# Optimization experiments

Measured on AMD Instinct MI355X. Metric: run time of the kernel, lower is better.

Reference implementation:

```python
import jax, jax.numpy as jnp
import numpy as np
from jax import lax

N_LAYERS = 10  # Sinkhorn(n_layers=10)


def setup_inputs() -> dict:
    key = jax.random.key(0)
    k1, k2, k3 = jax.random.split(key, 3)
    S, NA, NB = 4, 4096, 4096
    alpha = jax.random.uniform(k1, (S, NA), jnp.float32, 0.05, 1.0)
    alpha = alpha / alpha.sum(-1, keepdims=True)  # probability simplex
    beta = jax.random.uniform(k2, (S, NB), jnp.float32, 0.05, 1.0)
    beta = beta / beta.sum(-1, keepdims=True)
    C = jax.random.uniform(k3, (NA, NB), jnp.float32)  # nonneg cost matrix
    eps = jnp.float32(0.1)  # entropic regularization
    return {"alpha": alpha, "beta": beta, "C": C, "eps": eps}


def reference(alpha, beta, C, eps):
    # Log-domain Sinkhorn: f,g are dual potentials, shapes (S,NA)/(S,NB).
    log_alpha = jnp.log(alpha)
    log_beta = jnp.log(beta)

    def log_dot_exp(A, b):
        # A: (n, m), b: (S, m) -> (S, n); matches torch log_dot_exp (2D case)
        return jax.scipy.special.logsumexp((-A[None, :, :] + b[:, None, :]) / eps, axis=-1)

    def step(carry, _):
        _, g = carry
        f = eps * (log_alpha - log_dot_exp(C, g))
        g = eps * (log_beta - log_dot_exp(C.T, f))
        return (f, g), None

    f0 = jnp.zeros_like(alpha)
    g0 = jnp.zeros_like(beta)
    (f, g), _ = lax.scan(step, (f0, g0), None, length=N_LAYERS)
    return f, g
```

## Files before the change

### kernel.cpp

```cpp
#include <hip/hip_runtime.h>
#include <stdint.h>

#define NN 4096
#define NITER 10
#define ROWS 16
#define NBLK 256

#define STG_OFF  131072
#define RED_OFF  147712

static __device__ __forceinline__ unsigned short f2bf(float f) {
  union { float f; unsigned int i; } x; x.f = f;
  unsigned int i = x.i;
  i += 0x7FFFu + ((i >> 16) & 1u);
  return (unsigned short)(i >> 16);
}
static __device__ __forceinline__ unsigned int pk2(float a, float b) {
  return (unsigned int)f2bf(a) | ((unsigned int)f2bf(b) << 16);
}
static __device__ __forceinline__ float2 unpk(unsigned int u) {
  union { unsigned int i; float f; } a, b;
  a.i = u << 16; b.i = u & 0xFFFF0000u;
  return make_float2(a.f, b.f);
}
static __device__ __forceinline__ float read_eps(const void* p) {
  float f = *(const float*)p;
  if (f > 1e-4f && f < 1.0f) return f;
  union { unsigned int i; float f; } x;
  x.i = ((unsigned int)*(const unsigned short*)p) << 16;
  return x.f;
}
static __device__ __forceinline__ void astore8(unsigned long long* p, unsigned long long v) {
  __hip_atomic_store(p, v, __ATOMIC_RELAXED, __HIP_MEMORY_SCOPE_AGENT);
}
static __device__ __forceinline__ float4 up4(unsigned int w0, unsigned int w1) {
  float2 a = unpk(w0), b = unpk(w1);
  return make_float4(a.x, a.y, b.x, b.y);
}

__global__ __launch_bounds__(256) void zero_flags(unsigned int* __restrict__ c) {
#pragma unroll
  for (int k = 0; k < 16; ++k) c[threadIdx.x + k * 256] = 0;
}

static __device__ __forceinline__ void grid_barrier(
    unsigned int* flags, int b, unsigned token) {
  __syncthreads();
  const int t = threadIdx.x;
  if (t == 0)
    __hip_atomic_store(flags + b * 16, token, __ATOMIC_RELAXED,
                       __HIP_MEMORY_SCOPE_AGENT);
  if (t < 64) {
    for (;;) {
      unsigned a0 = __hip_atomic_load(flags + t * 16,          __ATOMIC_RELAXED, __HIP_MEMORY_SCOPE_AGENT);
      unsigned a1 = __hip_atomic_load(flags + (t + 64) * 16,   __ATOMIC_RELAXED, __HIP_MEMORY_SCOPE_AGENT);
      unsigned a2 = __hip_atomic_load(flags + (t + 128) * 16,  __ATOMIC_RELAXED, __HIP_MEMORY_SCOPE_AGENT);
      unsigned a3 = __hip_atomic_load(flags + (t + 192) * 16,  __ATOMIC_RELAXED, __HIP_MEMORY_SCOPE_AGENT);
      bool ok = a0 >= token && a1 >= token && a2 >= token && a3 >= token;
      if (__ballot(ok) == 0xFFFFFFFFFFFFFFFFull) break;
      __builtin_amdgcn_s_sleep(2);
    }
  }
  __syncthreads();
}

__global__ __launch_bounds__(256, 1) void sinkhorn_all(
    const float* __restrict__ alpha, const float* __restrict__ beta,
    const float* __restrict__ C, const void* __restrict__ epsp,
    unsigned short* __restrict__ K, unsigned long long* __restrict__ u_ep,
    unsigned long long* __restrict__ v_ep, unsigned int* __restrict__ flags,
    float* __restrict__ out) {
  __shared__ float4 smem4[9488];
  char* sm = (char*)smem4;
  const int t = threadIdx.x, b = blockIdx.x;
  const int wave = t >> 6, lane = t & 63, sw = lane & 7;
  const int own = ((b & 7) << 5) | (b >> 3);
  const int base0 = own * ROWS;
  const float eps = read_eps(epsp);
  const float nie = -1.0f / eps;
  unsigned tok = 0;

#pragma unroll 2
  for (int r = 0; r < ROWS; ++r) {
    const float4* Crow = (const float4*)(C + (size_t)(base0 + r) * NN) + t * 4;
    float4 c0 = Crow[0], c1 = Crow[1], c2 = Crow[2], c3 = Crow[3];
    uint4 k0, k1;
    k0.x = pk2(__expf(c0.x * nie), __expf(c0.y * nie));
    k0.y = pk2(__expf(c0.z * nie), __expf(c0.w * nie));
    k0.z = pk2(__expf(c1.x * nie), __expf(c1.y * nie));
    k0.w = pk2(__expf(c1.z * nie), __expf(c1.w * nie));
    k1.x = pk2(__expf(c2.x * nie), __expf(c2.y * nie));
    k1.y = pk2(__expf(c2.z * nie), __expf(c2.w * nie));
    k1.z = pk2(__expf(c3.x * nie), __expf(c3.y * nie));
    k1.w = pk2(__expf(c3.z * nie), __expf(c3.w * nie));
    uint4* Krow = (uint4*)(K + (size_t)(base0 + r) * NN);
    Krow[t * 2] = k0;
    Krow[t * 2 + 1] = k1;
  }

  {
    const int p = t & 3;
    const int rb = t >> 2;
    const int cb = p * 4;
#pragma unroll 1
    for (int q = 0; q < 64; q += 8) {
      float4 cv[8];
#pragma unroll
      for (int z = 0; z < 8; ++z)
        cv[z] = *(const float4*)(C + (size_t)((q + z) * 64 + rb) * NN + base0 + cb);
#pragma unroll
      for (int z = 0; z < 8; ++z) {
        int n = (q + z) * 64 + rb;
        int u16 = ((n >> 10) * 8 + ((n >> 3) & 7)) * 256 + ((n >> 6) & 15) * 16;
        int jo = (n & 7) * 2;
        *(unsigned short*)(sm + (size_t)(u16 + cb + 0) * 16 + jo) = f2bf(__expf(cv[z].x * nie));
        *(unsigned short*)(sm + (size_t)(u16 + cb + 1) * 16 + jo) = f2bf(__expf(cv[z].y * nie));
        *(unsigned short*)(sm + (size_t)(u16 + cb + 2) * 16 + jo) = f2bf(__expf(cv[z].z * nie));
        *(unsigned short*)(sm + (size_t)(u16 + cb + 3) * 16 + jo) = f2bf(__expf(cv[z].w * nie));
      }
    }
  }

  for (int it = 0; it < NITER; ++it) {
    float acc[4][4] = {};
    const int r0 = base0 + wave * 4;
    const uint4* Kr0 = (const uint4*)(K + (size_t)r0 * NN);
    const uint4* VB = (const uint4*)(v_ep + (size_t)(it - 1) * NN);
    uint4 sv0, sv1;
    if (it > 0) { sv0 = VB[t * 2]; sv1 = VB[t * 2 + 1]; }
#pragma unroll 1
    for (int q = 0; q < 4; ++q) {
      {
        float4* L = (float4*)(sm + STG_OFF);
        int s0 = t * 4;
        if (it == 0) {
          float4 one = make_float4(1.f, 1.f, 1.f, 1.f);
#pragma unroll
          for (int e = 0; e < 4; ++e) {
            int s = s0 + e;
            L[s ^ ((s >> 3) & 7)] = one;
          }
        } else {
          float4 f0 = up4(sv0.x, sv0.y), f1 = up4(sv0.z, sv0.w);
          float4 f2 = up4(sv1.x, sv1.y), f3 = up4(sv1.z, sv1.w);
          L[(s0 + 0) ^ (((s0 + 0) >> 3) & 7)] = f0;
          L[(s0 + 1) ^ (((s0 + 1) >> 3) & 7)] = f1;
          L[(s0 + 2) ^ (((s0 + 2) >> 3) & 7)] = f2;
          L[(s0 + 3) ^ (((s0 + 3) >> 3) & 7)] = f3;
        }
      }
      __syncthreads();
      if (it > 0 && q < 3) {
        sv0 = VB[(q + 1) * 512 + t * 2];
        sv1 = VB[(q + 1) * 512 + t * 2 + 1];
      }
      uint4 karr[8];
#pragma unroll
      for (int ms = 0; ms < 2; ++ms) {
        int moff = q * 128 + ms * 64 + lane;
        karr[ms * 4 + 0] = Kr0[moff];
        karr[ms * 4 + 1] = Kr0[moff + 512];
        karr[ms * 4 + 2] = Kr0[moff + 1024];
        karr[ms * 4 + 3] = Kr0[moff + 1536];
      }
      const float4* VL = (const float4*)(sm + STG_OFF);
#pragma unroll
      for (int ms = 0; ms < 2; ++ms) {
        int mb = ms * 512 + lane * 8;
        float4 vv[8];
#pragma unroll
        for (int j = 0; j < 8; ++j) vv[j] = VL[mb + (j ^ sw)];
#pragma unroll
        for (int r = 0; r < 4; ++r) {
          unsigned int cw[4] = {karr[ms*4+r].x, karr[ms*4+r].y,
                                karr[ms*4+r].z, karr[ms*4+r].w};
#pragma unroll
          for (int w = 0; w < 4; ++w) {
            float2 f = unpk(cw[w]);
            float4 va = vv[2 * w], vb = vv[2 * w + 1];
            acc[r][0] += f.x * va.x; acc[r][1] += f.x * va.y;
            acc[r][2] += f.x * va.z; acc[r][3] += f.x * va.w;
            acc[r][0] += f.y * vb.x; acc[r][1] += f.y * vb.y;
            acc[r][2] += f.y * vb.z; acc[r][3] += f.y * vb.w;
          }
        }
      }
      __syncthreads();
    }
#pragma unroll
    for (int off = 32; off > 0; off >>= 1)
#pragma unroll
      for (int r = 0; r < 4; ++r)
#pragma unroll
        for (int s = 0; s < 4; ++s)
          acc[r][s] += __shfl_xor(acc[r][s], off);
    if (lane < 4) {
      int row = r0 + lane;
      float ux = alpha[0 * NN + row] / acc[lane][0];
      float uy = alpha[1 * NN + row] / acc[lane][1];
      float uz = alpha[2 * NN + row] / acc[lane][2];
      float uw = alpha[3 * NN + row] / acc[lane][3];
      unsigned long long ub = (unsigned long long)pk2(ux, uy) |
                              ((unsigned long long)pk2(uz, uw) << 32);
      astore8(u_ep + (size_t)it * NN + row, ub);
      if (it == NITER - 1) {
        out[0 * NN + row] = eps * __logf(ux);
        out[1 * NN + row] = eps * __logf(uy);
        out[2 * NN + row] = eps * __logf(uz);
        out[3 * NN + row] = eps * __logf(uw);
      }
    }
    grid_barrier(flags, b, ++tok);

    float4 bacc = make_float4(0.f, 0.f, 0.f, 0.f);
    const uint4* UB = (const uint4*)(u_ep + (size_t)it * NN);
    uint4 su0 = UB[t * 2], su1 = UB[t * 2 + 1];
#pragma unroll 1
    for (int q = 0; q < 4; ++q) {
      {
        char* US = sm + STG_OFF;
        int n0 = t * 4;
        float4 f0 = up4(su0.x, su0.y), f1 = up4(su0.z, su0.w);
        float4 f2 = up4(su1.x, su1.y), f3 = up4(su1.z, su1.w);
        *(float4*)(US + (n0 + 0) * 16 + ((n0 + 0) >> 6) * 16) = f0;
        *(float4*)(US + (n0 + 1) * 16 + ((n0 + 1) >> 6) * 16) = f1;
        *(float4*)(US + (n0 + 2) * 16 + ((n0 + 2) >> 6) * 16) = f2;
        *(float4*)(US + (n0 + 3) * 16 + ((n0 + 3) >> 6) * 16) = f3;
      }
      __syncthreads();
      if (q < 3) {
        su0 = UB[(q + 1) * 512 + t * 2];
        su1 = UB[(q + 1) * 512 + t * 2 + 1];
      }
      const char* US = sm + STG_OFF;
      const int k = t >> 4;
#pragma unroll
      for (int i = 0; i < 8; ++i) {
        uint4 kt = ((const uint4*)sm)[(q * 8 + i) * 256 + t];
        int nb = k * 64 + i * 8;
        unsigned int kw[4] = {kt.x, kt.y, kt.z, kt.w};
#pragma unroll
        for (int w = 0; w < 4; ++w) {
          float2 f = unpk(kw[w]);
          int j0 = nb + 2 * w, j1 = nb + 2 * w + 1;
          float4 u0 = *(const float4*)(US + j0 * 16 + (j0 >> 6) * 16);
          float4 u1 = *(const float4*)(US + j1 * 16 + (j1 >> 6) * 16);
          bacc.x += f.x * u0.x; bacc.y += f.x * u0.y;
          bacc.z += f.x * u0.z; bacc.w += f.x * u0.w;
          bacc.x += f.y * u1.x; bacc.y += f.y * u1.y;
          bacc.z += f.y * u1.z; bacc.w += f.y * u1.w;
        }
      }
      __syncthreads();
    }
    {
      float4* red = (float4*)(sm + RED_OFF);
      red[(t >> 4) * 16 + (t & 15)] = bacc;
    }
    __syncthreads();
    if (t < 16) {
      const float4* red = (const float4*)(sm + RED_OFF);
      float4 a = make_float4(0.f, 0.f, 0.f, 0.f);
#pragma unroll
      for (int k2 = 0; k2 < 16; ++k2) {
        float4 r = red[k2 * 16 + t];
        a.x += r.x; a.y += r.y; a.z += r.z; a.w += r.w;
      }
      int m = base0 + t;
      float vx = beta[0 * NN + m] / a.x;
      float vy = beta[1 * NN + m] / a.y;
      float vz = beta[2 * NN + m] / a.z;
      float vw = beta[3 * NN + m] / a.w;
      unsigned long long vb = (unsigned long long)pk2(vx, vy) |
                              ((unsigned long long)pk2(vz, vw) << 32);
      astore8(v_ep + (size_t)it * NN + m, vb);
      if (it == NITER - 1) {
        out[4 * NN + 0 * NN + m] = eps * __logf(vx);
        out[4 * NN + 1 * NN + m] = eps * __logf(vy);
        out[4 * NN + 2 * NN + m] = eps * __logf(vz);
        out[4 * NN + 3 * NN + m] = eps * __logf(vw);
      }
    }
    if (it < NITER - 1) grid_barrier(flags, b, ++tok);
  }
}

extern "C" void kernel_launch(void* const* d_in, const int* in_sizes, int n_in,
                              void* d_out, int out_size, void* d_ws, size_t ws_size,
                              hipStream_t stream) {
  (void)in_sizes; (void)n_in; (void)out_size; (void)ws_size;
  const float* alpha = (const float*)d_in[0];
  const float* beta  = (const float*)d_in[1];
  const float* C     = (const float*)d_in[2];
  const void*  epsp  = d_in[3];

  char* ws = (char*)d_ws;
  unsigned short* K        = (unsigned short*)ws;
  unsigned long long* u_ep = (unsigned long long*)(ws + 33554432);
  unsigned long long* v_ep = (unsigned long long*)(ws + 33554432 + 327680);
  unsigned int* flags      = (unsigned int*)(ws + 33554432 + 655360);
  float* out = (float*)d_out;

  zero_flags<<<1, 256, 0, stream>>>(flags);
  sinkhorn_all<<<NBLK, 256, 0, stream>>>(alpha, beta, C, epsp, K, u_ep, v_ep,
                                         flags, out);
}
```

Before: 268.0 us.

## Replace grid barriers with per-element readiness polling and packed FMAs

```diff
diff --git a/kernel.cpp b/kernel.cpp
--- a/kernel.cpp
+++ b/kernel.cpp
@@ -7,7 +7,9 @@
 #define NBLK 256
 
 #define STG_OFF  131072
-#define RED_OFF  147712
+#define RED_OFF  149504
+
+typedef float v2f __attribute__((ext_vector_type(2)));
 
 static __device__ __forceinline__ unsigned short f2bf(float f) {
   union { float f; unsigned int i; } x; x.f = f;
@@ -30,6 +32,9 @@
   x.i = ((unsigned int)*(const unsigned short*)p) << 16;
   return x.f;
 }
+static __device__ __forceinline__ unsigned long long aload8(const unsigned long long* p) {
+  return __hip_atomic_load(p, __ATOMIC_RELAXED, __HIP_MEMORY_SCOPE_AGENT);
+}
 static __device__ __forceinline__ void astore8(unsigned long long* p, unsigned long long v) {
   __hip_atomic_store(p, v, __ATOMIC_RELAXED, __HIP_MEMORY_SCOPE_AGENT);
 }
@@ -37,40 +42,23 @@
   float2 a = unpk(w0), b = unpk(w1);
   return make_float4(a.x, a.y, b.x, b.y);
 }
-
-__global__ __launch_bounds__(256) void zero_flags(unsigned int* __restrict__ c) {
-#pragma unroll
-  for (int k = 0; k < 16; ++k) c[threadIdx.x + k * 256] = 0;
-}
-
-static __device__ __forceinline__ void grid_barrier(
-    unsigned int* flags, int b, unsigned token) {
-  __syncthreads();
-  const int t = threadIdx.x;
-  if (t == 0)
-    __hip_atomic_store(flags + b * 16, token, __ATOMIC_RELAXED,
-                       __HIP_MEMORY_SCOPE_AGENT);
-  if (t < 64) {
-    for (;;) {
-      unsigned a0 = __hip_atomic_load(flags + t * 16,          __ATOMIC_RELAXED, __HIP_MEMORY_SCOPE_AGENT);
-      unsigned a1 = __hip_atomic_load(flags + (t + 64) * 16,   __ATOMIC_RELAXED, __HIP_MEMORY_SCOPE_AGENT);
-      unsigned a2 = __hip_atomic_load(flags + (t + 128) * 16,  __ATOMIC_RELAXED, __HIP_MEMORY_SCOPE_AGENT);
-      unsigned a3 = __hip_atomic_load(flags + (t + 192) * 16,  __ATOMIC_RELAXED, __HIP_MEMORY_SCOPE_AGENT);
-      bool ok = a0 >= token && a1 >= token && a2 >= token && a3 >= token;
-      if (__ballot(ok) == 0xFFFFFFFFFFFFFFFFull) break;
-      __builtin_amdgcn_s_sleep(2);
-    }
-  }
-  __syncthreads();
-}
+static __device__ __forceinline__ bool bad8(unsigned long long x) {
+  unsigned lo = (unsigned)x, hi = (unsigned)(x >> 32);
+  if ((lo | hi) & 0x80008000u) return true;
+  return ((lo & 0xffffu) == 0u) || ((lo >> 16) == 0u) ||
+         ((hi & 0xffffu) == 0u) || ((hi >> 16) == 0u);
+}
+static __device__ __forceinline__ v2f mk2(float a, float b) {
+  v2f r; r.x = a; r.y = b; return r;
+}
+#define FMA2(a, b, c) __builtin_elementwise_fma(a, b, c)
 
 __global__ __launch_bounds__(256, 1) void sinkhorn_all(
     const float* __restrict__ alpha, const float* __restrict__ beta,
     const float* __restrict__ C, const void* __restrict__ epsp,
     unsigned short* __restrict__ K, unsigned long long* __restrict__ u_ep,
-    unsigned long long* __restrict__ v_ep, unsigned int* __restrict__ flags,
-    float* __restrict__ out) {
-  __shared__ float4 smem4[9488];
+    unsigned long long* __restrict__ v_ep, float* __restrict__ out) {
+  __shared__ float4 smem4[9600];
   char* sm = (char*)smem4;
   const int t = threadIdx.x, b = blockIdx.x;
   const int wave = t >> 6, lane = t & 63, sw = lane & 7;
@@ -78,7 +66,6 @@
   const int base0 = own * ROWS;
   const float eps = read_eps(epsp);
   const float nie = -1.0f / eps;
-  unsigned tok = 0;
 
 #pragma unroll 2
   for (int r = 0; r < ROWS; ++r) {
@@ -99,9 +86,7 @@
   }
 
   {
-    const int p = t & 3;
-    const int rb = t >> 2;
-    const int cb = p * 4;
+    const int p = t & 3, rb = t >> 2, cb = p * 4;
 #pragma unroll 1
     for (int q = 0; q < 64; q += 8) {
       float4 cv[8];
@@ -122,12 +107,9 @@
   }
 
   for (int it = 0; it < NITER; ++it) {
-    float acc[4][4] = {};
+    v2f acc01[4] = {}, acc23[4] = {};
     const int r0 = base0 + wave * 4;
     const uint4* Kr0 = (const uint4*)(K + (size_t)r0 * NN);
-    const uint4* VB = (const uint4*)(v_ep + (size_t)(it - 1) * NN);
-    uint4 sv0, sv1;
-    if (it > 0) { sv0 = VB[t * 2]; sv1 = VB[t * 2 + 1]; }
 #pragma unroll 1
     for (int q = 0; q < 4; ++q) {
       {
@@ -141,8 +123,18 @@
             L[s ^ ((s >> 3) & 7)] = one;
           }
         } else {
-          float4 f0 = up4(sv0.x, sv0.y), f1 = up4(sv0.z, sv0.w);
-          float4 f2 = up4(sv1.x, sv1.y), f3 = up4(sv1.z, sv1.w);
+          const unsigned long long* P = v_ep + (size_t)(it - 1) * NN + q * 1024 + t * 4;
+          unsigned long long a0, a1, a2, a3;
+          for (;;) {
+            a0 = aload8(P); a1 = aload8(P + 1);
+            a2 = aload8(P + 2); a3 = aload8(P + 3);
+            if (!(bad8(a0) || bad8(a1) || bad8(a2) || bad8(a3))) break;
+            __builtin_amdgcn_s_sleep(1);
+          }
+          float4 f0 = up4((unsigned)a0, (unsigned)(a0 >> 32));
+          float4 f1 = up4((unsigned)a1, (unsigned)(a1 >> 32));
+          float4 f2 = up4((unsigned)a2, (unsigned)(a2 >> 32));
+          float4 f3 = up4((unsigned)a3, (unsigned)(a3 >> 32));
           L[(s0 + 0) ^ (((s0 + 0) >> 3) & 7)] = f0;
           L[(s0 + 1) ^ (((s0 + 1) >> 3) & 7)] = f1;
           L[(s0 + 2) ^ (((s0 + 2) >> 3) & 7)] = f2;
@@ -150,10 +142,6 @@
         }
       }
       __syncthreads();
-      if (it > 0 && q < 3) {
-        sv0 = VB[(q + 1) * 512 + t * 2];
-        sv1 = VB[(q + 1) * 512 + t * 2 + 1];
-      }
       uint4 karr[8];
 #pragma unroll
       for (int ms = 0; ms < 2; ++ms) {
@@ -178,28 +166,34 @@
           for (int w = 0; w < 4; ++w) {
             float2 f = unpk(cw[w]);
             float4 va = vv[2 * w], vb = vv[2 * w + 1];
-            acc[r][0] += f.x * va.x; acc[r][1] += f.x * va.y;
-            acc[r][2] += f.x * va.z; acc[r][3] += f.x * va.w;
-            acc[r][0] += f.y * vb.x; acc[r][1] += f.y * vb.y;
-            acc[r][2] += f.y * vb.z; acc[r][3] += f.y * vb.w;
+            acc01[r] = FMA2(mk2(f.x, f.x), mk2(va.x, va.y), acc01[r]);
+            acc23[r] = FMA2(mk2(f.x, f.x), mk2(va.z, va.w), acc23[r]);
+            acc01[r] = FMA2(mk2(f.y, f.y), mk2(vb.x, vb.y), acc01[r]);
+            acc23[r] = FMA2(mk2(f.y, f.y), mk2(vb.z, vb.w), acc23[r]);
           }
         }
       }
       __syncthreads();
     }
+    float accf[4][4];
+#pragma unroll
+    for (int r = 0; r < 4; ++r) {
+      accf[r][0] = acc01[r].x; accf[r][1] = acc01[r].y;
+      accf[r][2] = acc23[r].x; accf[r][3] = acc23[r].y;
+    }
 #pragma unroll
     for (int off = 32; off > 0; off >>= 1)
 #pragma unroll
       for (int r = 0; r < 4; ++r)
 #pragma unroll
         for (int s = 0; s < 4; ++s)
-          acc[r][s] += __shfl_xor(acc[r][s], off);
+          accf[r][s] += __shfl_xor(accf[r][s], off);
     if (lane < 4) {
       int row = r0 + lane;
-      float ux = alpha[0 * NN + row] / acc[lane][0];
-      float uy = alpha[1 * NN + row] / acc[lane][1];
-      float uz = alpha[2 * NN + row] / acc[lane][2];
-      float uw = alpha[3 * NN + row] / acc[lane][3];
+      float ux = alpha[0 * NN + row] / accf[lane][0];
+      float uy = alpha[1 * NN + row] / accf[lane][1];
+      float uz = alpha[2 * NN + row] / accf[lane][2];
+      float uw = alpha[3 * NN + row] / accf[lane][3];
       unsigned long long ub = (unsigned long long)pk2(ux, uy) |
                               ((unsigned long long)pk2(uz, uw) << 32);
       astore8(u_ep + (size_t)it * NN + row, ub);
@@ -210,28 +204,31 @@
         out[3 * NN + row] = eps * __logf(uw);
       }
     }
-    grid_barrier(flags, b, ++tok);
-
-    float4 bacc = make_float4(0.f, 0.f, 0.f, 0.f);
-    const uint4* UB = (const uint4*)(u_ep + (size_t)it * NN);
-    uint4 su0 = UB[t * 2], su1 = UB[t * 2 + 1];
+
+    v2f bacc01 = {}, bacc23 = {};
 #pragma unroll 1
     for (int q = 0; q < 4; ++q) {
       {
         char* US = sm + STG_OFF;
+        const unsigned long long* P = u_ep + (size_t)it * NN + q * 1024 + t * 4;
+        unsigned long long a0, a1, a2, a3;
+        for (;;) {
+          a0 = aload8(P); a1 = aload8(P + 1);
+          a2 = aload8(P + 2); a3 = aload8(P + 3);
+          if (!(bad8(a0) || bad8(a1) || bad8(a2) || bad8(a3))) break;
+          __builtin_amdgcn_s_sleep(1);
+        }
+        float4 f0 = up4((unsigned)a0, (unsigned)(a0 >> 32));
+        float4 f1 = up4((unsigned)a1, (unsigned)(a1 >> 32));
+        float4 f2 = up4((unsigned)a2, (unsigned)(a2 >> 32));
+        float4 f3 = up4((unsigned)a3, (unsigned)(a3 >> 32));
         int n0 = t * 4;
-        float4 f0 = up4(su0.x, su0.y), f1 = up4(su0.z, su0.w);
-        float4 f2 = up4(su1.x, su1.y), f3 = up4(su1.z, su1.w);
-        *(float4*)(US + (n0 + 0) * 16 + ((n0 + 0) >> 6) * 16) = f0;
-        *(float4*)(US + (n0 + 1) * 16 + ((n0 + 1) >> 6) * 16) = f1;
-        *(float4*)(US + (n0 + 2) * 16 + ((n0 + 2) >> 6) * 16) = f2;
-        *(float4*)(US + (n0 + 3) * 16 + ((n0 + 3) >> 6) * 16) = f3;
+        *(float4*)(US + (n0 + 0) * 16 + ((n0 + 0) >> 3) * 16) = f0;
+        *(float4*)(US + (n0 + 1) * 16 + ((n0 + 1) >> 3) * 16) = f1;
+        *(float4*)(US + (n0 + 2) * 16 + ((n0 + 2) >> 3) * 16) = f2;
+        *(float4*)(US + (n0 + 3) * 16 + ((n0 + 3) >> 3) * 16) = f3;
       }
       __syncthreads();
-      if (q < 3) {
-        su0 = UB[(q + 1) * 512 + t * 2];
-        su1 = UB[(q + 1) * 512 + t * 2 + 1];
-      }
       const char* US = sm + STG_OFF;
       const int k = t >> 4;
 #pragma unroll
@@ -243,19 +240,20 @@
         for (int w = 0; w < 4; ++w) {
           float2 f = unpk(kw[w]);
           int j0 = nb + 2 * w, j1 = nb + 2 * w + 1;
-          float4 u0 = *(const float4*)(US + j0 * 16 + (j0 >> 6) * 16);
-          float4 u1 = *(const float4*)(US + j1 * 16 + (j1 >> 6) * 16);
-          bacc.x += f.x * u0.x; bacc.y += f.x * u0.y;
-          bacc.z += f.x * u0.z; bacc.w += f.x * u0.w;
-          bacc.x += f.y * u1.x; bacc.y += f.y * u1.y;
-          bacc.z += f.y * u1.z; bacc.w += f.y * u1.w;
+          float4 u0 = *(const float4*)(US + j0 * 16 + (j0 >> 3) * 16);
+          float4 u1 = *(const float4*)(US + j1 * 16 + (j1 >> 3) * 16);
+          bacc01 = FMA2(mk2(f.x, f.x), mk2(u0.x, u0.y), bacc01);
+          bacc23 = FMA2(mk2(f.x, f.x), mk2(u0.z, u0.w), bacc23);
+          bacc01 = FMA2(mk2(f.y, f.y), mk2(u1.x, u1.y), bacc01);
+          bacc23 = FMA2(mk2(f.y, f.y), mk2(u1.z, u1.w), bacc23);
         }
       }
       __syncthreads();
     }
     {
       float4* red = (float4*)(sm + RED_OFF);
-      red[(t >> 4) * 16 + (t & 15)] = bacc;
+      red[(t >> 4) * 16 + (t & 15)] =
+          make_float4(bacc01.x, bacc01.y, bacc23.x, bacc23.y);
     }
     __syncthreads();
     if (t < 16) {
@@ -281,7 +279,7 @@
         out[4 * NN + 3 * NN + m] = eps * __logf(vw);
       }
     }
-    if (it < NITER - 1) grid_barrier(flags, b, ++tok);
+    __syncthreads();
   }
 }
 
@@ -298,10 +296,8 @@
   unsigned short* K        = (unsigned short*)ws;
   unsigned long long* u_ep = (unsigned long long*)(ws + 33554432);
   unsigned long long* v_ep = (unsigned long long*)(ws + 33554432 + 327680);
-  unsigned int* flags      = (unsigned int*)(ws + 33554432 + 655360);
   float* out = (float*)d_out;
 
-  zero_flags<<<1, 256, 0, stream>>>(flags);
   sinkhorn_all<<<NBLK, 256, 0, stream>>>(alpha, beta, C, epsp, K, u_ep, v_ep,
-                                         flags, out);
-}
+                                         out);
+}
```

New measurement: 302.3 us. +12.8%, slower.
